# Optimization experiments

Measured on AMD Instinct MI355X. Metric: run time of the kernel, lower is better.

Reference implementation:

```python
import jax, jax.numpy as jnp
from jax import lax
import numpy as np

EPS = 1e-12  # matches torch F.normalize eps


def _dtw_similarity(s1, s2):
    # s1: [L1, D], s2: [L2, D]
    L1, L2 = s1.shape[0], s2.shape[0]
    s1n = s1 / jnp.maximum(jnp.linalg.norm(s1, axis=1, keepdims=True), EPS)
    s2n = s2 / jnp.maximum(jnp.linalg.norm(s2, axis=1, keepdims=True), EPS)
    dist = 1.0 - s1n @ s2n.T  # [L1, L2] cosine distance

    # DTW DP. Row 0 is a cumsum; each subsequent row has a left-to-right
    # sequential dependency handled by an inner scan.
    row0 = jnp.cumsum(dist[0])

    def row_step(prev_row, d_row):
        # prev_row: dtw[i-1, :], d_row: dist[i, :]
        first = prev_row[0] + d_row[0]  # dtw[i, 0]
        # min(prev[j], prev[j-1]) for j >= 1 (vectorized part of the min)
        p = jnp.minimum(prev_row[1:], prev_row[:-1])

        def col_step(c, inp):
            dj, pj = inp
            new = dj + jnp.minimum(pj, c)  # c = dtw[i, j-1]
            return new, new

        _, rest = lax.scan(col_step, first, (d_row[1:], p))
        new_row = jnp.concatenate([first[None], rest])
        return new_row, None

    last_row, _ = lax.scan(row_step, row0, dist[1:])
    dtw_distance = last_row[-1]
    normalized = dtw_distance / (L1 + L2)
    return 1.0 / (1.0 + normalized)


def setup_inputs() -> dict:
    key = jax.random.key(0)
    k1, k2 = jax.random.split(key)
    seq1 = jax.random.normal(k1, (16, 1024, 768), dtype=jnp.float32)
    seq2 = jax.random.normal(k2, (16, 1024, 768), dtype=jnp.float32)
    return {"seq1": seq1, "seq2": seq2}


def reference(seq1, seq2):
    # seq1: [B, L1, D], seq2: [B, L2, D] -> [B]
    return jax.vmap(_dtw_similarity)(seq1, seq2)
```

## Files before the change

### kernel.cpp

```cpp
#include <hip/hip_runtime.h>
#include <hip/hip_bf16.h>

typedef __attribute__((ext_vector_type(4))) float f32x4;
typedef __attribute__((ext_vector_type(8))) short bf16x8;

#define DINF 1e30f

__device__ __forceinline__ unsigned short f2bf(float f) {
    unsigned int u = __builtin_bit_cast(unsigned int, f);
    u += 0x7FFFu + ((u >> 16) & 1u);
    return (unsigned short)(u >> 16);
}

__global__ __launch_bounds__(256) void norm_bf16_kernel(
    const float* __restrict__ s1, const float* __restrict__ s2,
    __hip_bfloat16* __restrict__ o1, __hip_bfloat16* __restrict__ o2) {
    const int gb = blockIdx.x;
    const float* in;
    __hip_bfloat16* out;
    int rowbase;
    if (gb < 4096) { in = s1; out = o1; rowbase = gb * 4; }
    else           { in = s2; out = o2; rowbase = (gb - 4096) * 4; }
    const int wv = threadIdx.x >> 6;
    const int l  = threadIdx.x & 63;
    const int row = rowbase + wv;

    const float* rp = in + (size_t)row * 768 + l * 4;
    float4 x0 = *(const float4*)(rp);
    float4 x1 = *(const float4*)(rp + 256);
    float4 x2 = *(const float4*)(rp + 512);

    float s = x0.x*x0.x + x0.y*x0.y + x0.z*x0.z + x0.w*x0.w
            + x1.x*x1.x + x1.y*x1.y + x1.z*x1.z + x1.w*x1.w
            + x2.x*x2.x + x2.y*x2.y + x2.z*x2.z + x2.w*x2.w;
#pragma unroll
    for (int off = 32; off > 0; off >>= 1) s += __shfl_xor(s, off, 64);

    const float inv = 1.0f / fmaxf(sqrtf(s), 1e-12f);

    __hip_bfloat16* op = out + (size_t)row * 768 + l * 4;
    ushort4 o;
    o.x = f2bf(x0.x*inv); o.y = f2bf(x0.y*inv); o.z = f2bf(x0.z*inv); o.w = f2bf(x0.w*inv);
    *(ushort4*)(op) = o;
    o.x = f2bf(x1.x*inv); o.y = f2bf(x1.y*inv); o.z = f2bf(x1.z*inv); o.w = f2bf(x1.w*inv);
    *(ushort4*)(op + 256) = o;
    o.x = f2bf(x2.x*inv); o.y = f2bf(x2.y*inv); o.z = f2bf(x2.z*inv); o.w = f2bf(x2.w*inv);
    *(ushort4*)(op + 512) = o;
}

__global__ __launch_bounds__(256) void gemm_dist_kernel(
    const __hip_bfloat16* __restrict__ A, const __hip_bfloat16* __restrict__ B,
    float* __restrict__ dist) {
    __shared__ __hip_bfloat16 lA[128 * 64];
    __shared__ __hip_bfloat16 lB[128 * 64];

    const int blk  = blockIdx.x;
    const int b    = blk >> 6;
    const int tile = blk & 63;
    const int tm = tile >> 3, tn = tile & 7;
    const int tid  = threadIdx.x;
    const int lane = tid & 63, w = tid >> 6;
    const int lr = lane & 15, lg = lane >> 4;
    const int wm = w >> 1, wn = w & 1;

    const __hip_bfloat16* Ab = A + (size_t)b * (1024 * 768) + (size_t)(tm * 128) * 768;
    const __hip_bfloat16* Bb = B + (size_t)b * (1024 * 768) + (size_t)(tn * 128) * 768;

    const int srow = tid >> 3;
    const int scol = (tid & 7) * 8;

    f32x4 acc[4][4];
#pragma unroll
    for (int m = 0; m < 4; ++m)
#pragma unroll
        for (int n = 0; n < 4; ++n) acc[m][n] = (f32x4){0.f, 0.f, 0.f, 0.f};

    for (int k0 = 0; k0 < 768; k0 += 64) {
        float4 va[4], vb[4];
#pragma unroll
        for (int q = 0; q < 4; ++q) {
            va[q] = *(const float4*)(Ab + (size_t)(q * 32 + srow) * 768 + k0 + scol);
            vb[q] = *(const float4*)(Bb + (size_t)(q * 32 + srow) * 768 + k0 + scol);
        }
#pragma unroll
        for (int q = 0; q < 4; ++q) {
            *(float4*)&lA[q * 2048 + tid * 8] = va[q];
            *(float4*)&lB[q * 2048 + tid * 8] = vb[q];
        }
        __syncthreads();

#pragma unroll
        for (int ks = 0; ks < 64; ks += 32) {
            bf16x8 af[4], bfr[4];
#pragma unroll
            for (int m = 0; m < 4; ++m)
                af[m] = *(const bf16x8*)&lA[(wm * 64 + m * 16 + lr) * 64 + ks + lg * 8];
#pragma unroll
            for (int n = 0; n < 4; ++n)
                bfr[n] = *(const bf16x8*)&lB[(wn * 64 + n * 16 + lr) * 64 + ks + lg * 8];
#pragma unroll
            for (int m = 0; m < 4; ++m)
#pragma unroll
                for (int n = 0; n < 4; ++n)
                    acc[m][n] = __builtin_amdgcn_mfma_f32_16x16x32_bf16(af[m], bfr[n], acc[m][n], 0, 0, 0);
        }
        __syncthreads();
    }

    float* Drow = dist + (size_t)b * (1024 * 1024);
#pragma unroll
    for (int m = 0; m < 4; ++m)
#pragma unroll
        for (int n = 0; n < 4; ++n)
#pragma unroll
            for (int r = 0; r < 4; ++r) {
                const int row = tm * 128 + wm * 64 + m * 16 + lg * 4 + r;
                const int col = tn * 128 + wn * 64 + n * 16 + lr;
                Drow[(size_t)row * 1024 + col] = 1.0f - acc[m][n][r];
            }
}

__global__ __launch_bounds__(64) void dtw_dp_kernel(
    const float* __restrict__ dist, float* __restrict__ out) {
    const int b = blockIdx.x;
    const int t = threadIdx.x;
    const float* Db = dist + (size_t)b * (1024 * 1024) + t * 16;

    float pr[16];
#pragma unroll
    for (int j = 0; j < 16; ++j) pr[j] = DINF;
    float cprev = DINF;
    float dg    = DINF;

    auto LOAD = [&](float4 (&bf)[4], int k) {
        int r = k - t;
        r = r < 0 ? 0 : (r > 1023 ? 1023 : r);
        const float4* p = (const float4*)(Db + (size_t)r * 1024);
#pragma unroll
        for (int i = 0; i < 4; ++i) bf[i] = p[i];
    };

    auto STEP = [&](float4 (&bf)[4], int k) {
        const int r = k - t;
        const bool act = (r >= 0) && (r < 1024);
        float lin = __shfl_up(cprev, 1, 64);
        if (t == 0) lin = DINF;
        float d[16];
#pragma unroll
        for (int i = 0; i < 4; ++i) {
            d[4*i+0] = bf[i].x; d[4*i+1] = bf[i].y; d[4*i+2] = bf[i].z; d[4*i+3] = bf[i].w;
        }
        float c[16];
        float m0 = fminf(fminf(pr[0], dg), lin);
        if (t == 0 && r == 0) m0 = 0.0f;
        c[0] = d[0] + m0;
#pragma unroll
        for (int j = 1; j < 16; ++j)
            c[j] = d[j] + fminf(fminf(pr[j], pr[j-1]), c[j-1]);
        if (act) {
#pragma unroll
            for (int j = 0; j < 16; ++j) pr[j] = c[j];
            cprev = c[15];
        }
        dg = lin;
    };

    float4 b0[4], b1[4], b2[4], b3[4];
    LOAD(b0, 0); LOAD(b1, 1); LOAD(b2, 2); LOAD(b3, 3);

#pragma unroll 1
    for (int k = 0; k < 1088; k += 4) {
        STEP(b0, k);     LOAD(b0, k + 4);
        STEP(b1, k + 1); LOAD(b1, k + 5);
        STEP(b2, k + 2); LOAD(b2, k + 6);
        STEP(b3, k + 3); LOAD(b3, k + 7);
    }

    if (t == 63) out[b] = 1.0f / (1.0f + cprev * (1.0f / 2048.0f));
}

extern "C" void kernel_launch(void* const* d_in, const int* in_sizes, int n_in,
                              void* d_out, int out_size, void* d_ws, size_t ws_size,
                              hipStream_t stream) {
    const float* s1 = (const float*)d_in[0];
    const float* s2 = (const float*)d_in[1];
    float* out = (float*)d_out;

    char* ws = (char*)d_ws;
    __hip_bfloat16* Abf = (__hip_bfloat16*)(ws);
    __hip_bfloat16* Bbf = (__hip_bfloat16*)(ws + 25165824);
    float* dist = (float*)(ws + 50331648);

    norm_bf16_kernel<<<8192, 256, 0, stream>>>(s1, s2, Abf, Bbf);
    gemm_dist_kernel<<<16 * 64, 256, 0, stream>>>(Abf, Bbf, dist);
    dtw_dp_kernel<<<16, 64, 0, stream>>>(dist, out);
}
```

Measured before the change: 235.2 us.

## Use direct global-to-LDS loads, swizzle GEMM blocks, and re-skew the DTW wavefront

The GEMM now loads tiles straight from global memory into LDS with global_load_lds, so the register round trip is gone. It also remaps block indices so neighbouring blocks cover different batches or tiles, which changes cache locality. The DTW kernel changes the wavefront skew from one row per lane to two rows per lane and drops the active-lane predication. It deepens prefetch to eight outstanding row loads and adds an epilogue of extra steps. The skew relies on clamped rows and DINF sentinels staying correct, which carries a risk of subtle correctness issues at the boundaries.

```diff
diff --git a/kernel.cpp b/kernel.cpp
--- a/kernel.cpp
+++ b/kernel.cpp
@@ -48,13 +48,18 @@
     *(ushort4*)(op + 512) = o;
 }
 
+#define GLOAD_LDS16(g, l)                                                      \
+    __builtin_amdgcn_global_load_lds(                                          \
+        (const __attribute__((address_space(1))) void*)(g),                    \
+        (__attribute__((address_space(3))) void*)(l), 16, 0, 0)
+
 __global__ __launch_bounds__(256) void gemm_dist_kernel(
     const __hip_bfloat16* __restrict__ A, const __hip_bfloat16* __restrict__ B,
     float* __restrict__ dist) {
     __shared__ __hip_bfloat16 lA[128 * 64];
     __shared__ __hip_bfloat16 lB[128 * 64];
 
-    const int blk  = blockIdx.x;
+    const int blk  = (blockIdx.x & 7) * 128 + (blockIdx.x >> 3);
     const int b    = blk >> 6;
     const int tile = blk & 63;
     const int tm = tile >> 3, tn = tile & 7;
@@ -69,6 +74,9 @@
     const int srow = tid >> 3;
     const int scol = (tid & 7) * 8;
 
+    char* lAb = (char*)lA;
+    char* lBb = (char*)lB;
+
     f32x4 acc[4][4];
 #pragma unroll
     for (int m = 0; m < 4; ++m)
@@ -76,16 +84,12 @@
         for (int n = 0; n < 4; ++n) acc[m][n] = (f32x4){0.f, 0.f, 0.f, 0.f};
 
     for (int k0 = 0; k0 < 768; k0 += 64) {
-        float4 va[4], vb[4];
 #pragma unroll
         for (int q = 0; q < 4; ++q) {
-            va[q] = *(const float4*)(Ab + (size_t)(q * 32 + srow) * 768 + k0 + scol);
-            vb[q] = *(const float4*)(Bb + (size_t)(q * 32 + srow) * 768 + k0 + scol);
-        }
-#pragma unroll
-        for (int q = 0; q < 4; ++q) {
-            *(float4*)&lA[q * 2048 + tid * 8] = va[q];
-            *(float4*)&lB[q * 2048 + tid * 8] = vb[q];
+            GLOAD_LDS16(Ab + (size_t)(q * 32 + srow) * 768 + k0 + scol,
+                        lAb + q * 4096 + w * 1024);
+            GLOAD_LDS16(Bb + (size_t)(q * 32 + srow) * 768 + k0 + scol,
+                        lBb + q * 4096 + w * 1024);
         }
         __syncthreads();
 
@@ -120,63 +124,87 @@
             }
 }
 
+
+#define DECLB(N) float4 N##_0, N##_1, N##_2, N##_3
+
+#define LOADB(N, kk) do {                                                      \
+    int r_ = (kk) - 2 * t;                                                     \
+    r_ = r_ < 0 ? 0 : (r_ > 1023 ? 1023 : r_);                                 \
+    const float4* p_ = (const float4*)(Db + ((size_t)r_ << 10));               \
+    N##_0 = p_[0]; N##_1 = p_[1]; N##_2 = p_[2]; N##_3 = p_[3];                \
+} while (0)
+
+#define STEPBODY(N, E0EXPR) do {                                               \
+    float e0_ = (E0EXPR);                                                      \
+    float c0_  = N##_0.x + e0_;                                                \
+    float c1_  = N##_0.y + fminf(fminf(p1,  p0),  c0_);                        \
+    float c2_  = N##_0.z + fminf(fminf(p2,  p1),  c1_);                        \
+    float c3_  = N##_0.w + fminf(fminf(p3,  p2),  c2_);                        \
+    float c4_  = N##_1.x + fminf(fminf(p4,  p3),  c3_);                        \
+    float c5_  = N##_1.y + fminf(fminf(p5,  p4),  c4_);                        \
+    float c6_  = N##_1.z + fminf(fminf(p6,  p5),  c5_);                        \
+    float c7_  = N##_1.w + fminf(fminf(p7,  p6),  c6_);                        \
+    float c8_  = N##_2.x + fminf(fminf(p8,  p7),  c7_);                        \
+    float c9_  = N##_2.y + fminf(fminf(p9,  p8),  c8_);                        \
+    float c10_ = N##_2.z + fminf(fminf(p10, p9),  c9_);                        \
+    float c11_ = N##_2.w + fminf(fminf(p11, p10), c10_);                       \
+    float c12_ = N##_3.x + fminf(fminf(p12, p11), c11_);                       \
+    float c13_ = N##_3.y + fminf(fminf(p13, p12), c12_);                       \
+    float c14_ = N##_3.z + fminf(fminf(p14, p13), c13_);                       \
+    float c15_ = N##_3.w + fminf(fminf(p15, p14), c14_);                       \
+    p0=c0_; p1=c1_; p2=c2_; p3=c3_; p4=c4_; p5=c5_; p6=c6_; p7=c7_;            \
+    p8=c8_; p9=c9_; p10=c10_; p11=c11_; p12=c12_; p13=c13_; p14=c14_; p15=c15_;\
+    a3 = a2; a2 = a1;                                                          \
+    a1 = __shfl_up(c15_, 1, 64);                                               \
+    a1 = lane0 ? DINF : a1;                                                    \
+} while (0)
+
+#define STEPB(N)       STEPBODY(N, fminf(fminf(p0, a3), a2))
+#define STEPB_FIRST(N) STEPBODY(N, lane0 ? 0.0f : fminf(fminf(p0, a3), a2))
+
 __global__ __launch_bounds__(64) void dtw_dp_kernel(
     const float* __restrict__ dist, float* __restrict__ out) {
     const int b = blockIdx.x;
     const int t = threadIdx.x;
-    const float* Db = dist + (size_t)b * (1024 * 1024) + t * 16;
-
-    float pr[16];
-#pragma unroll
-    for (int j = 0; j < 16; ++j) pr[j] = DINF;
-    float cprev = DINF;
-    float dg    = DINF;
-
-    auto LOAD = [&](float4 (&bf)[4], int k) {
-        int r = k - t;
-        r = r < 0 ? 0 : (r > 1023 ? 1023 : r);
-        const float4* p = (const float4*)(Db + (size_t)r * 1024);
-#pragma unroll
-        for (int i = 0; i < 4; ++i) bf[i] = p[i];
-    };
-
-    auto STEP = [&](float4 (&bf)[4], int k) {
-        const int r = k - t;
-        const bool act = (r >= 0) && (r < 1024);
-        float lin = __shfl_up(cprev, 1, 64);
-        if (t == 0) lin = DINF;
-        float d[16];
-#pragma unroll
-        for (int i = 0; i < 4; ++i) {
-            d[4*i+0] = bf[i].x; d[4*i+1] = bf[i].y; d[4*i+2] = bf[i].z; d[4*i+3] = bf[i].w;
-        }
-        float c[16];
-        float m0 = fminf(fminf(pr[0], dg), lin);
-        if (t == 0 && r == 0) m0 = 0.0f;
-        c[0] = d[0] + m0;
-#pragma unroll
-        for (int j = 1; j < 16; ++j)
-            c[j] = d[j] + fminf(fminf(pr[j], pr[j-1]), c[j-1]);
-        if (act) {
-#pragma unroll
-            for (int j = 0; j < 16; ++j) pr[j] = c[j];
-            cprev = c[15];
-        }
-        dg = lin;
-    };
-
-    float4 b0[4], b1[4], b2[4], b3[4];
-    LOAD(b0, 0); LOAD(b1, 1); LOAD(b2, 2); LOAD(b3, 3);
+    const bool lane0 = (t == 0);
+    const float* Db = dist + ((size_t)b << 20) + t * 16;
+
+    float p0 = DINF, p1 = DINF, p2 = DINF, p3 = DINF,
+          p4 = DINF, p5 = DINF, p6 = DINF, p7 = DINF,
+          p8 = DINF, p9 = DINF, p10 = DINF, p11 = DINF,
+          p12 = DINF, p13 = DINF, p14 = DINF, p15 = DINF;
+    float a1 = DINF, a2 = DINF, a3 = DINF;
+
+    DECLB(A); DECLB(B); DECLB(C); DECLB(D);
+    DECLB(E); DECLB(F); DECLB(G); DECLB(H);
+
+    LOADB(A, 0); LOADB(B, 1); LOADB(C, 2); LOADB(D, 3);
+    LOADB(E, 4); LOADB(F, 5); LOADB(G, 6); LOADB(H, 7);
+
+    STEPB_FIRST(A); LOADB(A, 8);
+    STEPB(B); LOADB(B, 9);
+    STEPB(C); LOADB(C, 10);
+    STEPB(D); LOADB(D, 11);
+    STEPB(E); LOADB(E, 12);
+    STEPB(F); LOADB(F, 13);
+    STEPB(G); LOADB(G, 14);
+    STEPB(H); LOADB(H, 15);
 
 #pragma unroll 1
-    for (int k = 0; k < 1088; k += 4) {
-        STEP(b0, k);     LOAD(b0, k + 4);
-        STEP(b1, k + 1); LOAD(b1, k + 5);
-        STEP(b2, k + 2); LOAD(b2, k + 6);
-        STEP(b3, k + 3); LOAD(b3, k + 7);
+    for (int k = 8; k < 1144; k += 8) {
+        STEPB(A); LOADB(A, k + 8);
+        STEPB(B); LOADB(B, k + 9);
+        STEPB(C); LOADB(C, k + 10);
+        STEPB(D); LOADB(D, k + 11);
+        STEPB(E); LOADB(E, k + 12);
+        STEPB(F); LOADB(F, k + 13);
+        STEPB(G); LOADB(G, k + 14);
+        STEPB(H); LOADB(H, k + 15);
     }
 
-    if (t == 63) out[b] = 1.0f / (1.0f + cprev * (1.0f / 2048.0f));
+    STEPB(A); STEPB(B); STEPB(C); STEPB(D); STEPB(E); STEPB(F);
+
+    if (t == 63) out[b] = 1.0f / (1.0f + p15 * (1.0f / 2048.0f));
 }
 
 extern "C" void kernel_launch(void* const* d_in, const int* in_sizes, int n_in,
```

Measured after the change: 258.6 us. 10.0% more time.
